# Kernel tuning notes

Hardware: AMD Instinct MI355X
Metric: run time of the kernel (lower is better)

## Reference

```python
import jax, jax.numpy as jnp
import numpy as np

N = 20000      # atoms
E = 320000     # edges
F = 128        # node_size (hard-pinned by split(128) / expand to 384)
RBF = 20
RC = 5.0
ITERS = 3
NM = 64        # molecules in batch


def setup_inputs() -> dict:
    key = jax.random.key(0)
    ks = iter(jax.random.split(key, 64))
    def nrm(shape, scale=0.05):
        return jax.random.normal(next(ks), shape, dtype=jnp.float32) * scale
    inp = {}
    inp["z"] = jax.random.randint(next(ks), (N,), 0, 119)
    inp["graph"] = jax.random.randint(next(ks), (E, 2), 0, N)
    inp["edges_dist"] = jax.random.uniform(next(ks), (E,), minval=0.5, maxval=RC, dtype=jnp.float32)
    sense = jax.random.normal(next(ks), (E, 3), dtype=jnp.float32)
    inp["edges_sense"] = sense / jnp.linalg.norm(sense, axis=1, keepdims=True)
    inp["graph_idx"] = jnp.sort(jax.random.randint(next(ks), (N,), 0, NM))
    # parameters (stacked over ITERS message/update blocks)
    inp["emb"] = nrm((119, F), 1.0)
    inp["mw1"] = nrm((ITERS, F, F)); inp["mb1"] = nrm((ITERS, F))
    inp["mw2"] = nrm((ITERS, 3 * F, F)); inp["mb2"] = nrm((ITERS, 3 * F))
    inp["ew"] = nrm((ITERS, 3 * F, RBF)); inp["eb"] = nrm((ITERS, 3 * F))
    inp["uw"] = nrm((ITERS, F, F)); inp["vw"] = nrm((ITERS, F, F))
    inp["aw1"] = nrm((ITERS, F, 2 * F)); inp["ab1"] = nrm((ITERS, F))
    inp["aw2"] = nrm((ITERS, 3 * F, F)); inp["ab2"] = nrm((ITERS, 3 * F))
    inp["ow1"] = nrm((F, F)); inp["ob1"] = nrm((F,))
    inp["ow2"] = nrm((1, F)); inp["ob2"] = nrm((1,))
    return inp


def reference(z, graph, edges_dist, edges_sense, graph_idx,
              emb, mw1, mb1, mw2, mb2, ew, eb,
              uw, vw, aw1, ab1, aw2, ab2, ow1, ob1, ow2, ob2):
    src = graph[:, 0]   # scatter target (index_add index)
    dst = graph[:, 1]   # gather source (neighbour)
    s = emb[z]                                  # [N, F]
    v = jnp.zeros((N, 3, F), dtype=s.dtype)     # [N, 3, F]
    # edge-level precompute (same every iteration)
    n = jnp.arange(1, RBF + 1, dtype=jnp.float32)
    d = edges_dist[:, None]
    rbf = jnp.sin(n * jnp.pi * d / RC) / d                              # [E, RBF]
    cut = 0.5 * (jnp.cos(jnp.pi * edges_dist / RC) + 1.0) * (edges_dist < RC)  # [E]
    for i in range(ITERS):
        # --- Message block ---
        a = jax.nn.silu(s @ mw1[i].T + mb1[i]) @ mw2[i].T + mb2[i]      # [N, 3F]
        dist_rep = (rbf @ ew[i].T + eb[i]) * cut[:, None]               # [E, 3F]
        res = a[dst] * dist_rep                                         # [E, 3F]
        rv, rs, rd = res[:, :F], res[:, F:2 * F], res[:, 2 * F:]
        resv = v[dst] * rv[:, None, :] + edges_sense[:, :, None] * rd[:, None, :]  # [E,3,F]
        s = s + 2.0 * jax.ops.segment_sum(rs, src, num_segments=N)
        v = v + 2.0 * jax.ops.segment_sum(resv, src, num_segments=N)
        # --- Update block ---
        Uv = v @ uw[i].T                                                # [N,3,F]
        Vv = v @ vw[i].T
        h = jnp.concatenate([s, jnp.linalg.norm(Vv, axis=1)], axis=-1)  # [N, 2F]
        a2 = jax.nn.silu(h @ aw1[i].T + ab1[i]) @ aw2[i].T + ab2[i]     # [N, 3F]
        avv, asv, ass = a2[:, :F], a2[:, F:2 * F], a2[:, 2 * F:]
        s = s + ass + asv * jnp.sum(Uv * Vv, axis=1)
        v = v + avv[:, None, :] * Uv
    out = jax.nn.silu(s @ ow1.T + ob1) @ ow2.T + ob2                    # [N, 1]
    return jax.ops.segment_sum(out, graph_idx, num_segments=NM)         # [NM, 1]
```

## Files before the change

kernel.cpp:

```cpp
#include <hip/hip_runtime.h>
#include <math.h>

#define NN 20000
#define NE 320000
#define FD 128
#define RBFN 20
#define RC_ 5.0f
#define NITER 3
#define NMOL 64
#define F3 384
#define F2 256
#define PI_ 3.14159265358979323846f
#define KB 128
#define LPAD 8
#define SDS 392
#define BM2 32

typedef __attribute__((ext_vector_type(8))) short  bf16x8;
typedef __attribute__((ext_vector_type(4))) float  floatx4;
typedef unsigned short u16;
typedef unsigned int   u32;

__device__ __forceinline__ u16 f2b(float x) {
    union { float f; unsigned int u; } v; v.f = x;
    unsigned int u = v.u;
    return (u16)((u + 0x7fffu + ((u >> 16) & 1u)) >> 16);
}
__device__ __forceinline__ float b2f(u16 x) {
    union { unsigned int u; float f; } v; v.u = ((unsigned int)x) << 16;
    return v.f;
}
__device__ __forceinline__ float blo(u32 w) {
    union { unsigned int u; float f; } v; v.u = w << 16; return v.f;
}
__device__ __forceinline__ float bhi(u32 w) {
    union { unsigned int u; float f; } v; v.u = w & 0xffff0000u; return v.f;
}
__device__ __forceinline__ u32 pack2(float a, float b) {
    return (u32)f2b(a) | ((u32)f2b(b) << 16);
}

__global__ __launch_bounds__(256) void init_all_kernel(
    const float* s0, int n0, const float* s1, int n1, const float* s2, int n2,
    const float* s3, int n3, const float* s4, int n4, const float* s5, int n5,
    const float* s6, int n6, u16* __restrict__ wdst,
    const float* __restrict__ ew, u16* __restrict__ ewb,
    const int* __restrict__ z, const float* __restrict__ emb,
    float* __restrict__ s, u16* __restrict__ sbf,
    float* __restrict__ v_a, int* __restrict__ v_pk_i, int* __restrict__ cnt)
{
    int idx = blockIdx.x * 256 + threadIdx.x;
    if (idx < NN * F3) v_a[idx] = 0.f;
    if (idx < NN * F3 / 2) v_pk_i[idx] = 0;
    if (idx < NN) cnt[idx] = 0;
    if (idx < NN * FD) {
        int n = idx >> 7, f = idx & 127;
        float v = emb[z[n] * FD + f];
        s[idx] = v; sbf[idx] = f2b(v);
    }
    if (idx < NITER * F3 * 32) {
        int k = idx & 31;
        int row = idx >> 5;
        ewb[idx] = (k < RBFN) ? f2b(ew[row * RBFN + k]) : (u16)0;
    }
    {
        int w = idx;
        u16* dst = wdst;
        if (w < n0) { dst[w] = f2b(s0[w]); return; } w -= n0; dst += n0;
        if (w < n1) { dst[w] = f2b(s1[w]); return; } w -= n1; dst += n1;
        if (w < n2) { dst[w] = f2b(s2[w]); return; } w -= n2; dst += n2;
        if (w < n3) { dst[w] = f2b(s3[w]); return; } w -= n3; dst += n3;
        if (w < n4) { dst[w] = f2b(s4[w]); return; } w -= n4; dst += n4;
        if (w < n5) { dst[w] = f2b(s5[w]); return; } w -= n5; dst += n5;
        if (w < n6) { dst[w] = f2b(s6[w]); }
    }
}

__global__ __launch_bounds__(256) void csr_count_kernel(const int* __restrict__ graph,
    int* __restrict__ cnt)
{
    int e = blockIdx.x * 256 + threadIdx.x;
    if (e >= NE) return;
    atomicAdd(&cnt[graph[2 * e]], 1);
}

__global__ __launch_bounds__(1024) void csr_scan_kernel(const int* __restrict__ cnt,
    int* __restrict__ row_ptr, int* __restrict__ cursor)
{
    __shared__ int sd[1024];
    int tid = threadIdx.x;
    const int chunk = (NN + 1023) / 1024;
    int start = tid * chunk;
    int end = start + chunk; if (end > NN) end = NN;
    int sum = 0;
    for (int j = start; j < end; j++) sum += cnt[j];
    sd[tid] = sum;
    __syncthreads();
    for (int off = 1; off < 1024; off <<= 1) {
        int v = 0;
        if (tid >= off) v = sd[tid - off];
        __syncthreads();
        if (tid >= off) sd[tid] += v;
        __syncthreads();
    }
    int run = (tid == 0) ? 0 : sd[tid - 1];
    for (int j = start; j < end; j++) {
        row_ptr[j] = run;
        cursor[j]  = run;
        run += cnt[j];
    }
    if (tid == 0) row_ptr[NN] = NE;
}

__global__ __launch_bounds__(256) void csr_scatter_kernel(const int* __restrict__ graph,
    int* __restrict__ cursor, int* __restrict__ edge_list)
{
    int e = blockIdx.x * 256 + threadIdx.x;
    if (e >= NE) return;
    int p = atomicAdd(&cursor[graph[2 * e]], 1);
    edge_list[p] = e;
}

__global__ __launch_bounds__(256) void edge_stream_kernel(
    const int* __restrict__ edge_list, const int* __restrict__ graph,
    const float* __restrict__ dist, const float* __restrict__ sense,
    u16* __restrict__ rbf_bf, float* __restrict__ cut_p,
    float* __restrict__ sense_p, int* __restrict__ dst_p)
{
    int j = blockIdx.x * 256 + threadIdx.x;
    if (j >= NE) return;
    int e = edge_list[j];
    float d = dist[e];
    float inv = 1.f / d;
    float base = PI_ * d / RC_;
    float s1, c1;
    __sincosf(base, &s1, &c1);
    float twoc = c1 + c1;
    u16 tmp[32];
    float sprev = 0.f, scur = s1;
    #pragma unroll
    for (int k = 0; k < RBFN; k++) {
        tmp[k] = f2b(scur * inv);
        float snext = twoc * scur - sprev;
        sprev = scur; scur = snext;
    }
    #pragma unroll
    for (int k = RBFN; k < 32; k++) tmp[k] = 0;
    u16* rb = rbf_bf + (size_t)j * 32;
    #pragma unroll
    for (int x = 0; x < 32; x += 8)
        *(bf16x8*)&rb[x] = *(const bf16x8*)&tmp[x];
    cut_p[j] = 0.5f * (c1 + 1.f) * (d < RC_ ? 1.f : 0.f);
    dst_p[j] = graph[2 * e + 1];
    sense_p[3 * j + 0] = sense[3 * e + 0];
    sense_p[3 * j + 1] = sense[3 * e + 1];
    sense_p[3 * j + 2] = sense[3 * e + 2];
}

template<int K1, bool PACK>
__global__ __launch_bounds__(256) void mlp_kernel(const u16* __restrict__ A,
    const u16* __restrict__ W1, const float* __restrict__ b1,
    const u16* __restrict__ W2, const float* __restrict__ b2,
    u16* __restrict__ Ob, int M)
{
    __shared__ u16 As[64][KB + LPAD];
    __shared__ u16 Ws[128][KB + LPAD];
    u16 (*T)[KB + LPAD] = &Ws[64];
    const int bm = blockIdx.x * 64;
    const int tid = threadIdx.x;
    const int wave = tid >> 6, lane = tid & 63;
    const int wm  = (wave >> 1) * 32;
    const int wn1 = (wave & 1) * 64;
    const int wn  = (wave & 1) * 32;
    const int quad = lane >> 4, lr = lane & 15;
    const int r = tid >> 2, q = tid & 3;

    floatx4 acc1[2][4];
    #pragma unroll
    for (int i = 0; i < 2; i++)
        #pragma unroll
        for (int j = 0; j < 4; j++) acc1[i][j] = (floatx4)0.f;

    for (int ko = 0; ko < K1; ko += KB) {
        {
            int gm = bm + r;
            u16* dA = &As[r][q * 32];
            if (gm < M) {
                const u16* ap = A + (size_t)gm * K1 + ko + q * 32;
                #pragma unroll
                for (int x = 0; x < 32; x += 8)
                    *(bf16x8*)&dA[x] = *(const bf16x8*)(ap + x);
            } else {
                #pragma unroll
                for (int x = 0; x < 32; x += 8)
                    *(bf16x8*)&dA[x] = (bf16x8)0;
            }
            #pragma unroll
            for (int h = 0; h < 2; h++) {
                int wr = r + h * 64;
                const u16* wp = W1 + (size_t)wr * K1 + ko + q * 32;
                u16* dW = &Ws[wr][q * 32];
                #pragma unroll
                for (int x = 0; x < 32; x += 8)
                    *(bf16x8*)&dW[x] = *(const bf16x8*)(wp + x);
            }
        }
        __syncthreads();
        #pragma unroll
        for (int kk = 0; kk < KB; kk += 32) {
            bf16x8 a0 = *(const bf16x8*)&As[wm + lr     ][kk + quad * 8];
            bf16x8 a1 = *(const bf16x8*)&As[wm + 16 + lr][kk + quad * 8];
            #pragma unroll
            for (int j = 0; j < 4; j++) {
                bf16x8 b = *(const bf16x8*)&Ws[wn1 + j * 16 + lr][kk + quad * 8];
                acc1[0][j] = __builtin_amdgcn_mfma_f32_16x16x32_bf16(a0, b, acc1[0][j], 0, 0, 0);
                acc1[1][j] = __builtin_amdgcn_mfma_f32_16x16x32_bf16(a1, b, acc1[1][j], 0, 0, 0);
            }
        }
        __syncthreads();
    }
    #pragma unroll
    for (int i = 0; i < 2; i++) {
        #pragma unroll
        for (int j = 0; j < 4; j++) {
            int col = wn1 + j * 16 + lr;
            float bb = b1[col];
            #pragma unroll
            for (int rr = 0; rr < 4; rr++) {
                int row = wm + i * 16 + quad * 4 + rr;
                float v = acc1[i][j][rr] + bb;
                v = v / (1.f + __expf(-v));
                T[row][col] = f2b(v);
            }
        }
    }

    for (int c0 = 0; c0 < F3; c0 += 64) {
        {
            const u16* wp = W2 + (size_t)(c0 + r) * KB + q * 32;
            u16* dW = &Ws[r][q * 32];
            #pragma unroll
            for (int x = 0; x < 32; x += 8)
                *(bf16x8*)&dW[x] = *(const bf16x8*)(wp + x);
        }
        __syncthreads();
        floatx4 acc2[2][2];
        #pragma unroll
        for (int i = 0; i < 2; i++)
            #pragma unroll
            for (int j = 0; j < 2; j++) acc2[i][j] = (floatx4)0.f;
        #pragma unroll
        for (int kk = 0; kk < KB; kk += 32) {
            bf16x8 a0 = *(const bf16x8*)&T[wm + lr     ][kk + quad * 8];
            bf16x8 a1 = *(const bf16x8*)&T[wm + 16 + lr][kk + quad * 8];
            bf16x8 b0 = *(const bf16x8*)&Ws[wn + lr     ][kk + quad * 8];
            bf16x8 b1 = *(const bf16x8*)&Ws[wn + 16 + lr][kk + quad * 8];
            acc2[0][0] = __builtin_amdgcn_mfma_f32_16x16x32_bf16(a0, b0, acc2[0][0], 0, 0, 0);
            acc2[0][1] = __builtin_amdgcn_mfma_f32_16x16x32_bf16(a0, b1, acc2[0][1], 0, 0, 0);
            acc2[1][0] = __builtin_amdgcn_mfma_f32_16x16x32_bf16(a1, b0, acc2[1][0], 0, 0, 0);
            acc2[1][1] = __builtin_amdgcn_mfma_f32_16x16x32_bf16(a1, b1, acc2[1][1], 0, 0, 0);
        }
        #pragma unroll
        for (int i = 0; i < 2; i++) {
            #pragma unroll
            for (int j = 0; j < 2; j++) {
                int gn = c0 + wn + j * 16 + lr;
                float bb = b2[gn];
                #pragma unroll
                for (int rr = 0; rr < 4; rr++) {
                    int gm = bm + wm + i * 16 + quad * 4 + rr;
                    if (gm < M) {
                        u16 val = f2b(acc2[i][j][rr] + bb);
                        if (PACK) {
                            int off = (gn < 256) ? ((gn & 127) * 2 + (gn >> 7))
                                                 : (256 + (gn & 127));
                            Ob[(size_t)gm * F3 + off] = val;
                        } else {
                            Ob[(size_t)gm * F3 + gn] = val;
                        }
                    }
                }
            }
        }
        __syncthreads();
    }
}

__global__ __launch_bounds__(256) void gemm_uv(const u16* __restrict__ A,
    const u16* __restrict__ Wu, const u16* __restrict__ Wv,
    u16* __restrict__ U, u16* __restrict__ V, int M)
{
    __shared__ u16 As[64][KB + LPAD];
    __shared__ u16 Bu[64][KB + LPAD];
    __shared__ u16 Bv[64][KB + LPAD];
    const int bm = blockIdx.x * 64;
    const int tid = threadIdx.x;
    const int r = tid >> 2;
    const int q = tid & 3;
    const int wave = tid >> 6;
    const int lane = tid & 63;
    const int wm = (wave >> 1) * 32;
    const int wn = (wave & 1) * 32;
    const int quad = lane >> 4;
    const int lr = lane & 15;

    {
        int gm = bm + r;
        u16* dA = &As[r][q * 32];
        if (gm < M) {
            const u16* ap = A + (size_t)gm * KB + q * 32;
            #pragma unroll
            for (int x = 0; x < 32; x += 8)
                *(bf16x8*)&dA[x] = *(const bf16x8*)(ap + x);
        } else {
            #pragma unroll
            for (int x = 0; x < 32; x += 8)
                *(bf16x8*)&dA[x] = (bf16x8)0;
        }
    }

    #pragma unroll
    for (int bn = 0; bn < FD; bn += 64) {
        {
            int gn = bn + r;
            const u16* up = Wu + (size_t)gn * KB + q * 32;
            const u16* vp = Wv + (size_t)gn * KB + q * 32;
            u16* dU = &Bu[r][q * 32];
            u16* dV = &Bv[r][q * 32];
            #pragma unroll
            for (int x = 0; x < 32; x += 8) {
                *(bf16x8*)&dU[x] = *(const bf16x8*)(up + x);
                *(bf16x8*)&dV[x] = *(const bf16x8*)(vp + x);
            }
        }
        __syncthreads();
        floatx4 au[2][2], av[2][2];
        #pragma unroll
        for (int i = 0; i < 2; i++)
            #pragma unroll
            for (int j = 0; j < 2; j++) { au[i][j] = (floatx4)0.f; av[i][j] = (floatx4)0.f; }
        #pragma unroll
        for (int kk = 0; kk < KB; kk += 32) {
            bf16x8 a0 = *(const bf16x8*)&As[wm + lr     ][kk + quad * 8];
            bf16x8 a1 = *(const bf16x8*)&As[wm + 16 + lr][kk + quad * 8];
            bf16x8 u0 = *(const bf16x8*)&Bu[wn + lr     ][kk + quad * 8];
            bf16x8 u1 = *(const bf16x8*)&Bu[wn + 16 + lr][kk + quad * 8];
            bf16x8 v0 = *(const bf16x8*)&Bv[wn + lr     ][kk + quad * 8];
            bf16x8 v1 = *(const bf16x8*)&Bv[wn + 16 + lr][kk + quad * 8];
            au[0][0] = __builtin_amdgcn_mfma_f32_16x16x32_bf16(a0, u0, au[0][0], 0, 0, 0);
            au[0][1] = __builtin_amdgcn_mfma_f32_16x16x32_bf16(a0, u1, au[0][1], 0, 0, 0);
            au[1][0] = __builtin_amdgcn_mfma_f32_16x16x32_bf16(a1, u0, au[1][0], 0, 0, 0);
            au[1][1] = __builtin_amdgcn_mfma_f32_16x16x32_bf16(a1, u1, au[1][1], 0, 0, 0);
            av[0][0] = __builtin_amdgcn_mfma_f32_16x16x32_bf16(a0, v0, av[0][0], 0, 0, 0);
            av[0][1] = __builtin_amdgcn_mfma_f32_16x16x32_bf16(a0, v1, av[0][1], 0, 0, 0);
            av[1][0] = __builtin_amdgcn_mfma_f32_16x16x32_bf16(a1, v0, av[1][0], 0, 0, 0);
            av[1][1] = __builtin_amdgcn_mfma_f32_16x16x32_bf16(a1, v1, av[1][1], 0, 0, 0);
        }
        #pragma unroll
        for (int i = 0; i < 2; i++) {
            #pragma unroll
            for (int j = 0; j < 2; j++) {
                int gn = bn + wn + j * 16 + lr;
                #pragma unroll
                for (int rr = 0; rr < 4; rr++) {
                    int gm = bm + wm + i * 16 + quad * 4 + rr;
                    if (gm < M) {
                        U[(size_t)gm * FD + gn] = f2b(au[i][j][rr]);
                        V[(size_t)gm * FD + gn] = f2b(av[i][j][rr]);
                    }
                }
            }
        }
        __syncthreads();
    }
}

__global__ __launch_bounds__(256) void edge_mfma_kernel(
    const u16* __restrict__ rbf_bf, const float* __restrict__ cut_p,
    const float* __restrict__ sense_p, const int* __restrict__ dst_p,
    const u16* __restrict__ ewb, const float* __restrict__ eb,
    const u16* __restrict__ a_pk, const float* __restrict__ s_in,
    const float* __restrict__ v_in, const u16* __restrict__ v_pk,
    const int* __restrict__ row_ptr,
    float* __restrict__ s_out, u16* __restrict__ s_obf,
    float* __restrict__ v_out, u16* __restrict__ v_obf)
{
    __shared__ u16   sdrep[16 * SDS];
    __shared__ float scut[16];
    __shared__ float ssen[16][4];
    __shared__ int   sdst[16];
    __shared__ float red[4 * 128];

    const int n = blockIdx.x;
    const int tid = threadIdx.x;
    const int wave = tid >> 6;
    const int lane = tid & 63;
    const int quad = lane >> 4;
    const int lr = lane & 15;
    const int f = tid & 127;
    const int half = tid >> 7;

    int beg = row_ptr[n], end = row_ptr[n + 1];
    float accs = 0.f, accv0 = 0.f, accv1 = 0.f, accv2 = 0.f;

    for (int t0 = beg; t0 < end; t0 += 16) {
        int cnt = end - t0; if (cnt > 16) cnt = 16;
        __syncthreads();
        if (tid < 16) {
            scut[tid] = (tid < cnt) ? cut_p[t0 + tid] : 0.f;
            sdst[tid] = (tid < cnt) ? dst_p[t0 + tid] : 0;
        }
        if (tid >= 64 && tid < 64 + 3 * cnt) {
            int x = tid - 64;
            ssen[x / 3][x % 3] = sense_p[3 * t0 + x];
        }
        bf16x8 afrag;
        int ge = t0 + lr;
        if (ge < end) afrag = *(const bf16x8*)&rbf_bf[(size_t)ge * 32 + quad * 8];
        else          afrag = (bf16x8)0;
        floatx4 dacc[6];
        #pragma unroll
        for (int nt = 0; nt < 6; nt++) {
            int nrow = (wave * 6 + nt) * 16 + lr;
            bf16x8 bfrag = *(const bf16x8*)&ewb[(size_t)nrow * 32 + quad * 8];
            dacc[nt] = __builtin_amdgcn_mfma_f32_16x16x32_bf16(afrag, bfrag, (floatx4)0.f, 0, 0, 0);
        }
        __syncthreads();
        #pragma unroll
        for (int nt = 0; nt < 6; nt++) {
            int ncol = (wave * 6 + nt) * 16 + lr;
            float ebn = eb[ncol];
            #pragma unroll
            for (int rr = 0; rr < 4; rr++) {
                int e = quad * 4 + rr;
                sdrep[e * SDS + ncol] = f2b((dacc[nt][rr] + ebn) * scut[e]);
            }
        }
        __syncthreads();
        int nh = cnt - half * 8; if (nh > 8) nh = 8;
        for (int k = 0; k < nh; k++) {
            int e = half * 8 + k;
            int dst = sdst[e];
            const u16* sr = &sdrep[e * SDS];
            float drv = b2f(sr[f]);
            float drs = b2f(sr[FD + f]);
            float drd = b2f(sr[2 * FD + f]);
            const u16* ar = a_pk + (size_t)dst * F3;
            u32 ap = *(const u32*)(ar + f * 2);
            float rv = b2f((u16)(ap & 0xffff)) * drv;
            float rs = b2f((u16)(ap >> 16))    * drs;
            float rd = b2f(ar[256 + f])        * drd;
            accs += rs;
            const u16* vr = v_pk + (size_t)dst * F3;
            u32 vp = *(const u32*)(vr + f * 2);
            accv0 += b2f((u16)(vp & 0xffff)) * rv + ssen[e][0] * rd;
            accv1 += b2f((u16)(vp >> 16))    * rv + ssen[e][1] * rd;
            accv2 += b2f(vr[256 + f])        * rv + ssen[e][2] * rd;
        }
    }
    __syncthreads();
    if (half == 1) {
        red[f] = accs; red[128 + f] = accv0; red[256 + f] = accv1; red[384 + f] = accv2;
    }
    __syncthreads();
    if (half == 0) {
        accs  += red[f];       accv0 += red[128 + f];
        accv1 += red[256 + f]; accv2 += red[384 + f];
        int nb = n * FD + f;
        float so = s_in[nb] + 2.f * accs;
        s_out[nb] = so; s_obf[nb] = f2b(so);
        int vb = n * F3 + f;
        float w0 = v_in[vb]           + 2.f * accv0;
        float w1 = v_in[vb + FD]      + 2.f * accv1;
        float w2 = v_in[vb + 2 * FD]  + 2.f * accv2;
        v_out[vb]          = w0; v_obf[vb]          = f2b(w0);
        v_out[vb + FD]     = w1; v_obf[vb + FD]     = f2b(w1);
        v_out[vb + 2 * FD] = w2; v_obf[vb + 2 * FD] = f2b(w2);
    }
}

template<bool LAST>
__global__ __launch_bounds__(256) void mlp2_update_next_kernel(
    const u16* __restrict__ sbf_mid, const float* __restrict__ s_mid,
    const float* __restrict__ v_mid,
    const u16* __restrict__ Uv, const u16* __restrict__ Vv,
    const u16* __restrict__ W1, const float* __restrict__ b1,
    const u16* __restrict__ W2, const float* __restrict__ b2,
    float* __restrict__ s_out,
    float* __restrict__ v_out, u16* __restrict__ v_pk,
    const u16* __restrict__ N_W1, const float* __restrict__ N_b1,
    const u16* __restrict__ N_W2, const float* __restrict__ N_b2,
    u16* __restrict__ a_pk,
    const u16* __restrict__ H_W1, const float* __restrict__ H_b1,
    const float* __restrict__ ow2, const float* __restrict__ ob2,
    float* __restrict__ nodeval, int M)
{
    __shared__ u16 As[BM2][KB + LPAD];
    __shared__ u16 Ws[128][KB + LPAD];
    u16 (*T)[KB + LPAD] = &Ws[64];
    const int bm = blockIdx.x * BM2;
    const int tid = threadIdx.x;
    const int wave = tid >> 6, lane = tid & 63;
    const int wrow = (wave >> 1) * 16;
    const int wn1  = (wave & 1) * 64;
    const int wn   = (wave & 1) * 32;
    const int quad = lane >> 4, lr = lane & 15;
    const int r = tid >> 2, q = tid & 3;
    const int r3 = tid >> 3, c16 = (tid & 7) * 16;

    floatx4 acc1[4];
    #pragma unroll
    for (int j = 0; j < 4; j++) acc1[j] = (floatx4)0.f;

    {
        int gm = bm + r3;
        u16* dA = &As[r3][c16];
        if (gm < M) {
            const u16* ap = sbf_mid + (size_t)gm * FD + c16;
            *(bf16x8*)&dA[0] = *(const bf16x8*)(ap);
            *(bf16x8*)&dA[8] = *(const bf16x8*)(ap + 8);
        } else {
            *(bf16x8*)&dA[0] = (bf16x8)0;
            *(bf16x8*)&dA[8] = (bf16x8)0;
        }
        #pragma unroll
        for (int h = 0; h < 2; h++) {
            int wr = r + h * 64;
            const u16* wp = W1 + (size_t)wr * F2 + q * 32;
            u16* dW = &Ws[wr][q * 32];
            #pragma unroll
            for (int x = 0; x < 32; x += 8)
                *(bf16x8*)&dW[x] = *(const bf16x8*)(wp + x);
        }
    }
    __syncthreads();
    #pragma unroll
    for (int kk = 0; kk < KB; kk += 32) {
        bf16x8 a0 = *(const bf16x8*)&As[wrow + lr][kk + quad * 8];
        #pragma unroll
        for (int j = 0; j < 4; j++) {
            bf16x8 b = *(const bf16x8*)&Ws[wn1 + j * 16 + lr][kk + quad * 8];
            acc1[j] = __builtin_amdgcn_mfma_f32_16x16x32_bf16(a0, b, acc1[j], 0, 0, 0);
        }
    }
    __syncthreads();
    {
        int gm = bm + r3;
        u16* dA = &As[r3][c16];
        if (gm < M) {
            const u16* vvp = Vv + (size_t)gm * F3 + c16;
            #pragma unroll
            for (int t = 0; t < 2; t++) {
                bf16x8 c0 = *(const bf16x8*)(vvp + t * 8);
                bf16x8 c1 = *(const bf16x8*)(vvp + FD + t * 8);
                bf16x8 c2 = *(const bf16x8*)(vvp + 2 * FD + t * 8);
                #pragma unroll
                for (int x = 0; x < 8; x++) {
                    float a = b2f((u16)c0[x]);
                    float b = b2f((u16)c1[x]);
                    float c = b2f((u16)c2[x]);
                    dA[t * 8 + x] = f2b(sqrtf(a * a + b * b + c * c));
                }
            }
        } else {
            *(bf16x8*)&dA[0] = (bf16x8)0;
            *(bf16x8*)&dA[8] = (bf16x8)0;
        }
        #pragma unroll
        for (int h = 0; h < 2; h++) {
            int wr = r + h * 64;
            const u16* wp = W1 + (size_t)wr * F2 + KB + q * 32;
            u16* dW = &Ws[wr][q * 32];
            #pragma unroll
            for (int x = 0; x < 32; x += 8)
                *(bf16x8*)&dW[x] = *(const bf16x8*)(wp + x);
        }
    }
    __syncthreads();
    #pragma unroll
    for (int kk = 0; kk < KB; kk += 32) {
        bf16x8 a0 = *(const bf16x8*)&As[wrow + lr][kk + quad * 8];
        #pragma unroll
        for (int j = 0; j < 4; j++) {
            bf16x8 b = *(const bf16x8*)&Ws[wn1 + j * 16 + lr][kk + quad * 8];
            acc1[j] = __builtin_amdgcn_mfma_f32_16x16x32_bf16(a0, b, acc1[j], 0, 0, 0);
        }
    }
    __syncthreads();
    #pragma unroll
    for (int j = 0; j < 4; j++) {
        int col = wn1 + j * 16 + lr;
        float bb = b1[col];
        #pragma unroll
        for (int rr = 0; rr < 4; rr++) {
            int row = wrow + quad * 4 + rr;
            float v = acc1[j][rr] + bb;
            v = v / (1.f + __expf(-v));
            T[row][col] = f2b(v);
        }
    }

    float avvr[2][4], asvr[2][4];
    #pragma unroll
    for (int pp = 0; pp < 6; pp++) {
        const int part  = pp / 3;
        const int piece = pp % 3;
        const int c0 = piece * 128 + part * 64;
        {
            const u16* wp = W2 + (size_t)(c0 + r) * KB + q * 32;
            u16* dW = &Ws[r][q * 32];
            #pragma unroll
            for (int x = 0; x < 32; x += 8)
                *(bf16x8*)&dW[x] = *(const bf16x8*)(wp + x);
        }
        __syncthreads();
        floatx4 acc2[2];
        #pragma unroll
        for (int j = 0; j < 2; j++) acc2[j] = (floatx4)0.f;
        #pragma unroll
        for (int kk = 0; kk < KB; kk += 32) {
            bf16x8 a0 = *(const bf16x8*)&T[wrow + lr][kk + quad * 8];
            bf16x8 b0 = *(const bf16x8*)&Ws[wn + lr     ][kk + quad * 8];
            bf16x8 b1 = *(const bf16x8*)&Ws[wn + 16 + lr][kk + quad * 8];
            acc2[0] = __builtin_amdgcn_mfma_f32_16x16x32_bf16(a0, b0, acc2[0], 0, 0, 0);
            acc2[1] = __builtin_amdgcn_mfma_f32_16x16x32_bf16(a0, b1, acc2[1], 0, 0, 0);
        }
        if (piece == 0) {
            #pragma unroll
            for (int j = 0; j < 2; j++) {
                int gn = c0 + wn + j * 16 + lr;
                float bb = b2[gn];
                #pragma unroll
                for (int rr = 0; rr < 4; rr++)
                    avvr[j][rr] = acc2[j][rr] + bb;
            }
        } else if (piece == 1) {
            #pragma unroll
            for (int j = 0; j < 2; j++) {
                int gn = c0 + wn + j * 16 + lr;
                float bb = b2[gn];
                #pragma unroll
                for (int rr = 0; rr < 4; rr++)
                    asvr[j][rr] = acc2[j][rr] + bb;
            }
        } else {
            #pragma unroll
            for (int j = 0; j < 2; j++) {
                int gn = c0 + wn + j * 16 + lr;
                int f  = gn - 256;
                float bb = b2[gn];
                #pragma unroll
                for (int rr = 0; rr < 4; rr++) {
                    int row = wrow + quad * 4 + rr;
                    int gm = bm + row;
                    if (gm < M) {
                        float ass = acc2[j][rr] + bb;
                        float asv = asvr[j][rr];
                        float avv = avvr[j][rr];
                        int vb = gm * F3 + f;
                        float u0 = b2f(Uv[vb]);
                        float u1 = b2f(Uv[vb + FD]);
                        float u2 = b2f(Uv[vb + 2 * FD]);
                        float w0 = b2f(Vv[vb]);
                        float w1 = b2f(Vv[vb + FD]);
                        float w2 = b2f(Vv[vb + 2 * FD]);
                        float dot = u0 * w0 + u1 * w1 + u2 * w2;
                        int nb = gm * FD + f;
                        float so = s_mid[nb] + ass + asv * dot;
                        s_out[nb] = so;
                        As[row][f] = f2b(so);
                        float y0 = v_mid[vb]          + avv * u0;
                        float y1 = v_mid[vb + FD]     + avv * u1;
                        float y2 = v_mid[vb + 2 * FD] + avv * u2;
                        v_out[vb]          = y0;
                        v_out[vb + FD]     = y1;
                        v_out[vb + 2 * FD] = y2;
                        char* vpb = (char*)v_pk + (size_t)gm * (2 * F3);
                        *(u32*)(vpb + 4 * f) = pack2(y0, y1);
                        *(u16*)(vpb + 512 + 2 * f) = f2b(y2);
                    } else {
                        As[row][f] = 0;
                    }
                }
            }
        }
        __syncthreads();
    }

    if constexpr (!LAST) {
        {
            #pragma unroll
            for (int h = 0; h < 2; h++) {
                int wr = r + h * 64;
                const u16* wp = N_W1 + (size_t)wr * KB + q * 32;
                u16* dW = &Ws[wr][q * 32];
                #pragma unroll
                for (int x = 0; x < 32; x += 8)
                    *(bf16x8*)&dW[x] = *(const bf16x8*)(wp + x);
            }
        }
        __syncthreads();
        #pragma unroll
        for (int j = 0; j < 4; j++) acc1[j] = (floatx4)0.f;
        #pragma unroll
        for (int kk = 0; kk < KB; kk += 32) {
            bf16x8 a0 = *(const bf16x8*)&As[wrow + lr][kk + quad * 8];
            #pragma unroll
            for (int j = 0; j < 4; j++) {
                bf16x8 b = *(const bf16x8*)&Ws[wn1 + j * 16 + lr][kk + quad * 8];
                acc1[j] = __builtin_amdgcn_mfma_f32_16x16x32_bf16(a0, b, acc1[j], 0, 0, 0);
            }
        }
        __syncthreads();
        #pragma unroll
        for (int j = 0; j < 4; j++) {
            int col = wn1 + j * 16 + lr;
            float bb = N_b1[col];
            #pragma unroll
            for (int rr = 0; rr < 4; rr++) {
                int row = wrow + quad * 4 + rr;
                float v = acc1[j][rr] + bb;
                v = v / (1.f + __expf(-v));
                T[row][col] = f2b(v);
            }
        }
        for (int pp = 0; pp < 6; pp++) {
            const int c0 = pp * 64;
            {
                const u16* wp = N_W2 + (size_t)(c0 + r) * KB + q * 32;
                u16* dW = &Ws[r][q * 32];
                #pragma unroll
                for (int x = 0; x < 32; x += 8)
                    *(bf16x8*)&dW[x] = *(const bf16x8*)(wp + x);
            }
            __syncthreads();
            floatx4 acc2[2];
            #pragma unroll
            for (int j = 0; j < 2; j++) acc2[j] = (floatx4)0.f;
            #pragma unroll
            for (int kk = 0; kk < KB; kk += 32) {
                bf16x8 a0 = *(const bf16x8*)&T[wrow + lr][kk + quad * 8];
                bf16x8 b0 = *(const bf16x8*)&Ws[wn + lr     ][kk + quad * 8];
                bf16x8 b1 = *(const bf16x8*)&Ws[wn + 16 + lr][kk + quad * 8];
                acc2[0] = __builtin_amdgcn_mfma_f32_16x16x32_bf16(a0, b0, acc2[0], 0, 0, 0);
                acc2[1] = __builtin_amdgcn_mfma_f32_16x16x32_bf16(a0, b1, acc2[1], 0, 0, 0);
            }
            #pragma unroll
            for (int j = 0; j < 2; j++) {
                int gn = c0 + wn + j * 16 + lr;
                float bb = N_b2[gn];
                #pragma unroll
                for (int rr = 0; rr < 4; rr++) {
                    int gm = bm + wrow + quad * 4 + rr;
                    if (gm < M) {
                        u16 val = f2b(acc2[j][rr] + bb);
                        int off = (gn < 256) ? ((gn & 127) * 2 + (gn >> 7))
                                             : (256 + (gn & 127));
                        a_pk[(size_t)gm * F3 + off] = val;
                    }
                }
            }
            __syncthreads();
        }
    } else {
        {
            #pragma unroll
            for (int h = 0; h < 2; h++) {
                int wr = r + h * 64;
                const u16* wp = H_W1 + (size_t)wr * KB + q * 32;
                u16* dW = &Ws[wr][q * 32];
                #pragma unroll
                for (int x = 0; x < 32; x += 8)
                    *(bf16x8*)&dW[x] = *(const bf16x8*)(wp + x);
            }
        }
        __syncthreads();
        #pragma unroll
        for (int j = 0; j < 4; j++) acc1[j] = (floatx4)0.f;
        #pragma unroll
        for (int kk = 0; kk < KB; kk += 32) {
            bf16x8 a0 = *(const bf16x8*)&As[wrow + lr][kk + quad * 8];
            #pragma unroll
            for (int j = 0; j < 4; j++) {
                bf16x8 b = *(const bf16x8*)&Ws[wn1 + j * 16 + lr][kk + quad * 8];
                acc1[j] = __builtin_amdgcn_mfma_f32_16x16x32_bf16(a0, b, acc1[j], 0, 0, 0);
            }
        }
        __syncthreads();
        float* ow2s = (float*)&As[0][0];
        if (tid < KB) ow2s[tid] = ow2[tid];
        #pragma unroll
        for (int j = 0; j < 4; j++) {
            int col = wn1 + j * 16 + lr;
            float bb = H_b1[col];
            #pragma unroll
            for (int rr = 0; rr < 4; rr++) {
                int row = wrow + quad * 4 + rr;
                float v = acc1[j][rr] + bb;
                v = v / (1.f + __expf(-v));
                T[row][col] = f2b(v);
            }
        }
        __syncthreads();
        int nl = tid >> 3, seg = tid & 7;
        float v = 0.f;
        #pragma unroll
        for (int x = 0; x < 16; x++) {
            int col = seg * 16 + x;
            v += b2f(T[nl][col]) * ow2s[col];
        }
        v += __shfl_down(v, 4);
        v += __shfl_down(v, 2);
        v += __shfl_down(v, 1);
        if (seg == 0) {
            int gm = bm + nl;
            if (gm < M) nodeval[gm] = v + ob2[0];
        }
    }
}

__global__ __launch_bounds__(1024) void mol_reduce_kernel(const float* __restrict__ nodeval,
    const int* __restrict__ gidx, float* __restrict__ out)
{
    __shared__ float mol[NMOL];
    int tid = threadIdx.x;
    if (tid < NMOL) mol[tid] = 0.f;
    __syncthreads();
    int cur = -1; float acc = 0.f;
    for (int x = tid; x < NN; x += 1024) {
        int g = gidx[x];
        float v = nodeval[x];
        if (g != cur) {
            if (cur >= 0) atomicAdd(&mol[cur], acc);
            cur = g; acc = v;
        } else acc += v;
    }
    if (cur >= 0) atomicAdd(&mol[cur], acc);
    __syncthreads();
    if (tid < NMOL) out[tid] = mol[tid];
}

extern "C" void kernel_launch(void* const* d_in, const int* in_sizes, int n_in,
                              void* d_out, int out_size, void* d_ws, size_t ws_size,
                              hipStream_t stream)
{
    const int*   z     = (const int*)d_in[0];
    const int*   graph = (const int*)d_in[1];
    const float* dist  = (const float*)d_in[2];
    const float* sense = (const float*)d_in[3];
    const int*   gidx  = (const int*)d_in[4];
    const float* emb   = (const float*)d_in[5];
    const float* mw1   = (const float*)d_in[6];
    const float* mb1   = (const float*)d_in[7];
    const float* mw2   = (const float*)d_in[8];
    const float* mb2   = (const float*)d_in[9];
    const float* ew    = (const float*)d_in[10];
    const float* eb    = (const float*)d_in[11];
    const float* uw    = (const float*)d_in[12];
    const float* vw    = (const float*)d_in[13];
    const float* aw1   = (const float*)d_in[14];
    const float* ab1   = (const float*)d_in[15];
    const float* aw2   = (const float*)d_in[16];
    const float* ab2   = (const float*)d_in[17];
    const float* ow1   = (const float*)d_in[18];
    const float* ob1   = (const float*)d_in[19];
    const float* ow2   = (const float*)d_in[20];
    const float* ob2   = (const float*)d_in[21];
    float* out = (float*)d_out;

    float* W = (float*)d_ws;
    float* s_a    = W; W += (size_t)NN * FD;
    float* s_b    = W; W += (size_t)NN * FD;
    float* v_a    = W; W += (size_t)NN * F3;
    float* v_b    = W; W += (size_t)NN * F3;
    float* cut_p  = W; W += (size_t)NE;
    float* sns_p  = W; W += (size_t)NE * 3;
    float* nodeval= W; W += (size_t)NN;
    u16* U = (u16*)W;
    u16* sbf_a = U; U += (size_t)NN * FD;
    u16* sbf_b = U; U += (size_t)NN * FD;
    u16* vbf_b = U; U += (size_t)NN * F3;
    u16* a_pk  = U; U += (size_t)NN * F3;
    u16* v_pk  = U; U += (size_t)NN * F3;
    u16* h_bf  = U; U += (size_t)NN * F2;
    u16* a2_bf = U; U += (size_t)NN * F3;
    u16* Uv_bf = U; U += (size_t)NN * F3;
    u16* Vv_bf = U; U += (size_t)NN * F3;
    u16* rbf_bf= U; U += (size_t)NE * 32;
    u16* ewb   = U; U += (size_t)NITER * F3 * 32;
    u16* wb    = U; U += 557056;
    int* ip = (int*)U;
    int* row_ptr   = ip; ip += NN + 1;
    int* cnt       = ip; ip += NN;
    int* cursor    = ip; ip += NN;
    int* edge_list = ip; ip += NE;
    int* dst_p     = ip; ip += NE;

    u16* wb_mw1 = wb;
    u16* wb_mw2 = wb + 49152;
    u16* wb_uw  = wb + 196608;
    u16* wb_vw  = wb + 245760;
    u16* wb_aw1 = wb + 294912;
    u16* wb_aw2 = wb + 393216;
    u16* wb_ow1 = wb + 540672;

    const int TB = 256;
    dim3 b256(TB);

    init_all_kernel<<<dim3((NN * F3 + TB - 1) / TB), b256, 0, stream>>>(
        mw1, 49152, mw2, 147456, uw, 49152, vw, 49152, aw1, 98304, aw2, 147456,
        ow1, 16384, wb, ew, ewb, z, emb, s_a, sbf_a, v_a, (int*)v_pk, cnt);
    csr_count_kernel<<<dim3((NE + TB - 1) / TB), b256, 0, stream>>>(graph, cnt);
    csr_scan_kernel<<<dim3(1), dim3(1024), 0, stream>>>(cnt, row_ptr, cursor);
    csr_scatter_kernel<<<dim3((NE + TB - 1) / TB), b256, 0, stream>>>(graph, cursor, edge_list);
    edge_stream_kernel<<<dim3((NE + TB - 1) / TB), b256, 0, stream>>>(
        edge_list, graph, dist, sense, rbf_bf, cut_p, sns_p, dst_p);

    dim3 gM((NN + 63) / 64);
    dim3 gM2((NN + BM2 - 1) / BM2);
    dim3 gUV((3 * NN + 63) / 64);

    mlp_kernel<128, true><<<gM, b256, 0, stream>>>(sbf_a,
        wb_mw1, mb1, wb_mw2, mb2, a_pk, NN);

    for (int i = 0; i < NITER; i++) {
        edge_mfma_kernel<<<dim3(NN), b256, 0, stream>>>(
            rbf_bf, cut_p, sns_p, dst_p,
            ewb + (size_t)i * F3 * 32, eb + (size_t)i * F3,
            a_pk, s_a, v_a, v_pk, row_ptr, s_b, sbf_b, v_b, vbf_b);
        gemm_uv<<<gUV, b256, 0, stream>>>(vbf_b, wb_uw + (size_t)i * FD * FD,
            wb_vw + (size_t)i * FD * FD, Uv_bf, Vv_bf, 3 * NN);
        if (i < NITER - 1) {
            mlp2_update_next_kernel<false><<<gM2, b256, 0, stream>>>(
                sbf_b, s_b, v_b, Uv_bf, Vv_bf,
                wb_aw1 + (size_t)i * FD * F2, ab1 + (size_t)i * FD,
                wb_aw2 + (size_t)i * F3 * FD, ab2 + (size_t)i * F3,
                s_a, v_a, v_pk,
                wb_mw1 + (size_t)(i + 1) * FD * FD, mb1 + (size_t)(i + 1) * FD,
                wb_mw2 + (size_t)(i + 1) * F3 * FD, mb2 + (size_t)(i + 1) * F3, a_pk,
                nullptr, nullptr, nullptr, nullptr, nullptr, NN);
        } else {
            mlp2_update_next_kernel<true><<<gM2, b256, 0, stream>>>(
                sbf_b, s_b, v_b, Uv_bf, Vv_bf,
                wb_aw1 + (size_t)i * FD * F2, ab1 + (size_t)i * FD,
                wb_aw2 + (size_t)i * F3 * FD, ab2 + (size_t)i * F3,
                s_a, v_a, v_pk,
                nullptr, nullptr, nullptr, nullptr, nullptr,
                wb_ow1, ob1, ow2, ob2, nodeval, NN);
        }
    }

    mol_reduce_kernel<<<dim3(1), dim3(1024), 0, stream>>>(nodeval, gidx, out);
}
```

Baseline: 855.1 us.

## Halve row tile in mlp1 and gemm_uv; fuse molecule reduction via atomics

The first MLP kernel and the U/V GEMM now use 32-row tiles instead of 64, so each wave covers 16 rows. That doubles the number of blocks and lowers per-block register and LDS use, at the cost of reloading weight tiles more often. The separate single-block molecule-reduction kernel is removed. The final update kernel now atomically adds each node's value into the output per molecule, with the output zeroed in the init kernel. This saves a launch and a serial reduction but adds per-node global atomics and makes the float summation order nondeterministic.

Measured after the change: 934.5 us. 9.3% more time.

```diff
diff --git a/kernel.cpp b/kernel.cpp
--- a/kernel.cpp
+++ b/kernel.cpp
@@ -47,12 +47,14 @@
     const float* __restrict__ ew, u16* __restrict__ ewb,
     const int* __restrict__ z, const float* __restrict__ emb,
     float* __restrict__ s, u16* __restrict__ sbf,
-    float* __restrict__ v_a, int* __restrict__ v_pk_i, int* __restrict__ cnt)
+    float* __restrict__ v_a, int* __restrict__ v_pk_i, int* __restrict__ cnt,
+    float* __restrict__ out)
 {
     int idx = blockIdx.x * 256 + threadIdx.x;
     if (idx < NN * F3) v_a[idx] = 0.f;
     if (idx < NN * F3 / 2) v_pk_i[idx] = 0;
     if (idx < NN) cnt[idx] = 0;
+    if (idx < NMOL) out[idx] = 0.f;
     if (idx < NN * FD) {
         int n = idx >> 7, f = idx & 127;
         float v = emb[z[n] * FD + f];
@@ -157,85 +159,74 @@
     sense_p[3 * j + 2] = sense[3 * e + 2];
 }
 
-template<int K1, bool PACK>
-__global__ __launch_bounds__(256) void mlp_kernel(const u16* __restrict__ A,
+__global__ __launch_bounds__(256) void mlp1_kernel(const u16* __restrict__ A,
     const u16* __restrict__ W1, const float* __restrict__ b1,
     const u16* __restrict__ W2, const float* __restrict__ b2,
     u16* __restrict__ Ob, int M)
 {
-    __shared__ u16 As[64][KB + LPAD];
+    __shared__ u16 As[BM2][KB + LPAD];
     __shared__ u16 Ws[128][KB + LPAD];
     u16 (*T)[KB + LPAD] = &Ws[64];
-    const int bm = blockIdx.x * 64;
+    const int bm = blockIdx.x * BM2;
     const int tid = threadIdx.x;
     const int wave = tid >> 6, lane = tid & 63;
-    const int wm  = (wave >> 1) * 32;
-    const int wn1 = (wave & 1) * 64;
-    const int wn  = (wave & 1) * 32;
+    const int wrow = (wave >> 1) * 16;
+    const int wn1  = (wave & 1) * 64;
+    const int wn   = (wave & 1) * 32;
     const int quad = lane >> 4, lr = lane & 15;
     const int r = tid >> 2, q = tid & 3;
-
-    floatx4 acc1[2][4];
-    #pragma unroll
-    for (int i = 0; i < 2; i++)
-        #pragma unroll
-        for (int j = 0; j < 4; j++) acc1[i][j] = (floatx4)0.f;
-
-    for (int ko = 0; ko < K1; ko += KB) {
-        {
-            int gm = bm + r;
-            u16* dA = &As[r][q * 32];
-            if (gm < M) {
-                const u16* ap = A + (size_t)gm * K1 + ko + q * 32;
-                #pragma unroll
-                for (int x = 0; x < 32; x += 8)
-                    *(bf16x8*)&dA[x] = *(const bf16x8*)(ap + x);
-            } else {
-                #pragma unroll
-                for (int x = 0; x < 32; x += 8)
-                    *(bf16x8*)&dA[x] = (bf16x8)0;
-            }
-            #pragma unroll
-            for (int h = 0; h < 2; h++) {
-                int wr = r + h * 64;
-                const u16* wp = W1 + (size_t)wr * K1 + ko + q * 32;
-                u16* dW = &Ws[wr][q * 32];
-                #pragma unroll
-                for (int x = 0; x < 32; x += 8)
-                    *(bf16x8*)&dW[x] = *(const bf16x8*)(wp + x);
-            }
-        }
-        __syncthreads();
-        #pragma unroll
-        for (int kk = 0; kk < KB; kk += 32) {
-            bf16x8 a0 = *(const bf16x8*)&As[wm + lr     ][kk + quad * 8];
-            bf16x8 a1 = *(const bf16x8*)&As[wm + 16 + lr][kk + quad * 8];
-            #pragma unroll
-            for (int j = 0; j < 4; j++) {
-                bf16x8 b = *(const bf16x8*)&Ws[wn1 + j * 16 + lr][kk + quad * 8];
-                acc1[0][j] = __builtin_amdgcn_mfma_f32_16x16x32_bf16(a0, b, acc1[0][j], 0, 0, 0);
-                acc1[1][j] = __builtin_amdgcn_mfma_f32_16x16x32_bf16(a1, b, acc1[1][j], 0, 0, 0);
-            }
-        }
-        __syncthreads();
-    }
-    #pragma unroll
-    for (int i = 0; i < 2; i++) {
+    const int r3 = tid >> 3, c16 = (tid & 7) * 16;
+
+    floatx4 acc1[4];
+    #pragma unroll
+    for (int j = 0; j < 4; j++) acc1[j] = (floatx4)0.f;
+
+    {
+        int gm = bm + r3;
+        u16* dA = &As[r3][c16];
+        if (gm < M) {
+            const u16* ap = A + (size_t)gm * KB + c16;
+            *(bf16x8*)&dA[0] = *(const bf16x8*)(ap);
+            *(bf16x8*)&dA[8] = *(const bf16x8*)(ap + 8);
+        } else {
+            *(bf16x8*)&dA[0] = (bf16x8)0;
+            *(bf16x8*)&dA[8] = (bf16x8)0;
+        }
+        #pragma unroll
+        for (int h = 0; h < 2; h++) {
+            int wr = r + h * 64;
+            const u16* wp = W1 + (size_t)wr * KB + q * 32;
+            u16* dW = &Ws[wr][q * 32];
+            #pragma unroll
+            for (int x = 0; x < 32; x += 8)
+                *(bf16x8*)&dW[x] = *(const bf16x8*)(wp + x);
+        }
+    }
+    __syncthreads();
+    #pragma unroll
+    for (int kk = 0; kk < KB; kk += 32) {
+        bf16x8 a0 = *(const bf16x8*)&As[wrow + lr][kk + quad * 8];
         #pragma unroll
         for (int j = 0; j < 4; j++) {
-            int col = wn1 + j * 16 + lr;
-            float bb = b1[col];
-            #pragma unroll
-            for (int rr = 0; rr < 4; rr++) {
-                int row = wm + i * 16 + quad * 4 + rr;
-                float v = acc1[i][j][rr] + bb;
-                v = v / (1.f + __expf(-v));
-                T[row][col] = f2b(v);
-            }
-        }
-    }
-
-    for (int c0 = 0; c0 < F3; c0 += 64) {
+            bf16x8 b = *(const bf16x8*)&Ws[wn1 + j * 16 + lr][kk + quad * 8];
+            acc1[j] = __builtin_amdgcn_mfma_f32_16x16x32_bf16(a0, b, acc1[j], 0, 0, 0);
+        }
+    }
+    __syncthreads();
+    #pragma unroll
+    for (int j = 0; j < 4; j++) {
+        int col = wn1 + j * 16 + lr;
+        float bb = b1[col];
+        #pragma unroll
+        for (int rr = 0; rr < 4; rr++) {
+            int row = wrow + quad * 4 + rr;
+            float v = acc1[j][rr] + bb;
+            v = v / (1.f + __expf(-v));
+            T[row][col] = f2b(v);
+        }
+    }
+    for (int pp = 0; pp < 6; pp++) {
+        const int c0 = pp * 64;
         {
             const u16* wp = W2 + (size_t)(c0 + r) * KB + q * 32;
             u16* dW = &Ws[r][q * 32];
@@ -244,41 +235,29 @@
                 *(bf16x8*)&dW[x] = *(const bf16x8*)(wp + x);
         }
         __syncthreads();
-        floatx4 acc2[2][2];
-        #pragma unroll
-        for (int i = 0; i < 2; i++)
-            #pragma unroll
-            for (int j = 0; j < 2; j++) acc2[i][j] = (floatx4)0.f;
+        floatx4 acc2[2];
+        #pragma unroll
+        for (int j = 0; j < 2; j++) acc2[j] = (floatx4)0.f;
         #pragma unroll
         for (int kk = 0; kk < KB; kk += 32) {
-            bf16x8 a0 = *(const bf16x8*)&T[wm + lr     ][kk + quad * 8];
-            bf16x8 a1 = *(const bf16x8*)&T[wm + 16 + lr][kk + quad * 8];
+            bf16x8 a0 = *(const bf16x8*)&T[wrow + lr][kk + quad * 8];
             bf16x8 b0 = *(const bf16x8*)&Ws[wn + lr     ][kk + quad * 8];
             bf16x8 b1 = *(const bf16x8*)&Ws[wn + 16 + lr][kk + quad * 8];
-            acc2[0][0] = __builtin_amdgcn_mfma_f32_16x16x32_bf16(a0, b0, acc2[0][0], 0, 0, 0);
-            acc2[0][1] = __builtin_amdgcn_mfma_f32_16x16x32_bf16(a0, b1, acc2[0][1], 0, 0, 0);
-            acc2[1][0] = __builtin_amdgcn_mfma_f32_16x16x32_bf16(a1, b0, acc2[1][0], 0, 0, 0);
-            acc2[1][1] = __builtin_amdgcn_mfma_f32_16x16x32_bf16(a1, b1, acc2[1][1], 0, 0, 0);
-        }
-        #pragma unroll
-        for (int i = 0; i < 2; i++) {
-            #pragma unroll
-            for (int j = 0; j < 2; j++) {
-                int gn = c0 + wn + j * 16 + lr;
-                float bb = b2[gn];
-                #pragma unroll
-                for (int rr = 0; rr < 4; rr++) {
-                    int gm = bm + wm + i * 16 + quad * 4 + rr;
-                    if (gm < M) {
-                        u16 val = f2b(acc2[i][j][rr] + bb);
-                        if (PACK) {
-                            int off = (gn < 256) ? ((gn & 127) * 2 + (gn >> 7))
-                                                 : (256 + (gn & 127));
-                            Ob[(size_t)gm * F3 + off] = val;
-                        } else {
-                            Ob[(size_t)gm * F3 + gn] = val;
-                        }
-                    }
+            acc2[0] = __builtin_amdgcn_mfma_f32_16x16x32_bf16(a0, b0, acc2[0], 0, 0, 0);
+            acc2[1] = __builtin_amdgcn_mfma_f32_16x16x32_bf16(a0, b1, acc2[1], 0, 0, 0);
+        }
+        #pragma unroll
+        for (int j = 0; j < 2; j++) {
+            int gn = c0 + wn + j * 16 + lr;
+            float bb = b2[gn];
+            #pragma unroll
+            for (int rr = 0; rr < 4; rr++) {
+                int gm = bm + wrow + quad * 4 + rr;
+                if (gm < M) {
+                    u16 val = f2b(acc2[j][rr] + bb);
+                    int off = (gn < 256) ? ((gn & 127) * 2 + (gn >> 7))
+                                         : (256 + (gn & 127));
+                    Ob[(size_t)gm * F3 + off] = val;
                 }
             }
         }
@@ -290,32 +269,31 @@
     const u16* __restrict__ Wu, const u16* __restrict__ Wv,
     u16* __restrict__ U, u16* __restrict__ V, int M)
 {
-    __shared__ u16 As[64][KB + LPAD];
+    __shared__ u16 As[BM2][KB + LPAD];
     __shared__ u16 Bu[64][KB + LPAD];
     __shared__ u16 Bv[64][KB + LPAD];
-    const int bm = blockIdx.x * 64;
+    const int bm = blockIdx.x * BM2;
     const int tid = threadIdx.x;
     const int r = tid >> 2;
     const int q = tid & 3;
+    const int r3 = tid >> 3, c16 = (tid & 7) * 16;
     const int wave = tid >> 6;
     const int lane = tid & 63;
-    const int wm = (wave >> 1) * 32;
+    const int wrow = (wave >> 1) * 16;
     const int wn = (wave & 1) * 32;
     const int quad = lane >> 4;
     const int lr = lane & 15;
 
     {
-        int gm = bm + r;
-        u16* dA = &As[r][q * 32];
+        int gm = bm + r3;
+        u16* dA = &As[r3][c16];
         if (gm < M) {
-            const u16* ap = A + (size_t)gm * KB + q * 32;
-            #pragma unroll
-            for (int x = 0; x < 32; x += 8)
-                *(bf16x8*)&dA[x] = *(const bf16x8*)(ap + x);
+            const u16* ap = A + (size_t)gm * KB + c16;
+            *(bf16x8*)&dA[0] = *(const bf16x8*)(ap);
+            *(bf16x8*)&dA[8] = *(const bf16x8*)(ap + 8);
         } else {
-            #pragma unroll
-            for (int x = 0; x < 32; x += 8)
-                *(bf16x8*)&dA[x] = (bf16x8)0;
+            *(bf16x8*)&dA[0] = (bf16x8)0;
+            *(bf16x8*)&dA[8] = (bf16x8)0;
         }
     }
 
@@ -334,40 +312,30 @@
             }
         }
         __syncthreads();
-        floatx4 au[2][2], av[2][2];
-        #pragma unroll
-        for (int i = 0; i < 2; i++)
-            #pragma unroll
-            for (int j = 0; j < 2; j++) { au[i][j] = (floatx4)0.f; av[i][j] = (floatx4)0.f; }
+        floatx4 au[2], av[2];
+        #pragma unroll
+        for (int j = 0; j < 2; j++) { au[j] = (floatx4)0.f; av[j] = (floatx4)0.f; }
         #pragma unroll
         for (int kk = 0; kk < KB; kk += 32) {
-            bf16x8 a0 = *(const bf16x8*)&As[wm + lr     ][kk + quad * 8];
-            bf16x8 a1 = *(const bf16x8*)&As[wm + 16 + lr][kk + quad * 8];
+            bf16x8 a0 = *(const bf16x8*)&As[wrow + lr][kk + quad * 8];
             bf16x8 u0 = *(const bf16x8*)&Bu[wn + lr     ][kk + quad * 8];
             bf16x8 u1 = *(const bf16x8*)&Bu[wn + 16 + lr][kk + quad * 8];
             bf16x8 v0 = *(const bf16x8*)&Bv[wn + lr     ][kk + quad * 8];
             bf16x8 v1 = *(const bf16x8*)&Bv[wn + 16 + lr][kk + quad * 8];
-            au[0][0] = __builtin_amdgcn_mfma_f32_16x16x32_bf16(a0, u0, au[0][0], 0, 0, 0);
-            au[0][1] = __builtin_amdgcn_mfma_f32_16x16x32_bf16(a0, u1, au[0][1], 0, 0, 0);
-            au[1][0] = __builtin_amdgcn_mfma_f32_16x16x32_bf16(a1, u0, au[1][0], 0, 0, 0);
-            au[1][1] = __builtin_amdgcn_mfma_f32_16x16x32_bf16(a1, u1, au[1][1], 0, 0, 0);
-            av[0][0] = __builtin_amdgcn_mfma_f32_16x16x32_bf16(a0, v0, av[0][0], 0, 0, 0);
-            av[0][1] = __builtin_amdgcn_mfma_f32_16x16x32_bf16(a0, v1, av[0][1], 0, 0, 0);
-            av[1][0] = __builtin_amdgcn_mfma_f32_16x16x32_bf16(a1, v0, av[1][0], 0, 0, 0);
-            av[1][1] = __builtin_amdgcn_mfma_f32_16x16x32_bf16(a1, v1, av[1][1], 0, 0, 0);
-        }
-        #pragma unroll
-        for (int i = 0; i < 2; i++) {
-            #pragma unroll
-            for (int j = 0; j < 2; j++) {
-                int gn = bn + wn + j * 16 + lr;
-                #pragma unroll
-                for (int rr = 0; rr < 4; rr++) {
-                    int gm = bm + wm + i * 16 + quad * 4 + rr;
-                    if (gm < M) {
-                        U[(size_t)gm * FD + gn] = f2b(au[i][j][rr]);
-                        V[(size_t)gm * FD + gn] = f2b(av[i][j][rr]);
-                    }
+            au[0] = __builtin_amdgcn_mfma_f32_16x16x32_bf16(a0, u0, au[0], 0, 0, 0);
+            au[1] = __builtin_amdgcn_mfma_f32_16x16x32_bf16(a0, u1, au[1], 0, 0, 0);
+            av[0] = __builtin_amdgcn_mfma_f32_16x16x32_bf16(a0, v0, av[0], 0, 0, 0);
+            av[1] = __builtin_amdgcn_mfma_f32_16x16x32_bf16(a0, v1, av[1], 0, 0, 0);
+        }
+        #pragma unroll
+        for (int j = 0; j < 2; j++) {
+            int gn = bn + wn + j * 16 + lr;
+            #pragma unroll
+            for (int rr = 0; rr < 4; rr++) {
+                int gm = bm + wrow + quad * 4 + rr;
+                if (gm < M) {
+                    U[(size_t)gm * FD + gn] = f2b(au[j][rr]);
+                    V[(size_t)gm * FD + gn] = f2b(av[j][rr]);
                 }
             }
         }
@@ -493,7 +461,7 @@
     u16* __restrict__ a_pk,
     const u16* __restrict__ H_W1, const float* __restrict__ H_b1,
     const float* __restrict__ ow2, const float* __restrict__ ob2,
-    float* __restrict__ nodeval, int M)
+    const int* __restrict__ gidx, float* __restrict__ outp, int M)
 {
     __shared__ u16 As[BM2][KB + LPAD];
     __shared__ u16 Ws[128][KB + LPAD];
@@ -814,30 +782,9 @@
         v += __shfl_down(v, 1);
         if (seg == 0) {
             int gm = bm + nl;
-            if (gm < M) nodeval[gm] = v + ob2[0];
-        }
-    }
-}
-
-__global__ __launch_bounds__(1024) void mol_reduce_kernel(const float* __restrict__ nodeval,
-    const int* __restrict__ gidx, float* __restrict__ out)
-{
-    __shared__ float mol[NMOL];
-    int tid = threadIdx.x;
-    if (tid < NMOL) mol[tid] = 0.f;
-    __syncthreads();
-    int cur = -1; float acc = 0.f;
-    for (int x = tid; x < NN; x += 1024) {
-        int g = gidx[x];
-        float v = nodeval[x];
-        if (g != cur) {
-            if (cur >= 0) atomicAdd(&mol[cur], acc);
-            cur = g; acc = v;
-        } else acc += v;
-    }
-    if (cur >= 0) atomicAdd(&mol[cur], acc);
-    __syncthreads();
-    if (tid < NMOL) out[tid] = mol[tid];
+            if (gm < M) atomicAdd(&outp[gidx[gm]], v + ob2[0]);
+        }
+    }
 }
 
 extern "C" void kernel_launch(void* const* d_in, const int* in_sizes, int n_in,
@@ -909,18 +856,17 @@
 
     init_all_kernel<<<dim3((NN * F3 + TB - 1) / TB), b256, 0, stream>>>(
         mw1, 49152, mw2, 147456, uw, 49152, vw, 49152, aw1, 98304, aw2, 147456,
-        ow1, 16384, wb, ew, ewb, z, emb, s_a, sbf_a, v_a, (int*)v_pk, cnt);
+        ow1, 16384, wb, ew, ewb, z, emb, s_a, sbf_a, v_a, (int*)v_pk, cnt, out);
     csr_count_kernel<<<dim3((NE + TB - 1) / TB), b256, 0, stream>>>(graph, cnt);
     csr_scan_kernel<<<dim3(1), dim3(1024), 0, stream>>>(cnt, row_ptr, cursor);
     csr_scatter_kernel<<<dim3((NE + TB - 1) / TB), b256, 0, stream>>>(graph, cursor, edge_list);
     edge_stream_kernel<<<dim3((NE + TB - 1) / TB), b256, 0, stream>>>(
         edge_list, graph, dist, sense, rbf_bf, cut_p, sns_p, dst_p);
 
-    dim3 gM((NN + 63) / 64);
     dim3 gM2((NN + BM2 - 1) / BM2);
-    dim3 gUV((3 * NN + 63) / 64);
-
-    mlp_kernel<128, true><<<gM, b256, 0, stream>>>(sbf_a,
+    dim3 gUV((3 * NN + BM2 - 1) / BM2);
+
+    mlp1_kernel<<<gM2, b256, 0, stream>>>(sbf_a,
         wb_mw1, mb1, wb_mw2, mb2, a_pk, NN);
 
     for (int i = 0; i < NITER; i++) {
@@ -938,7 +884,7 @@
                 s_a, v_a, v_pk,
                 wb_mw1 + (size_t)(i + 1) * FD * FD, mb1 + (size_t)(i + 1) * FD,
                 wb_mw2 + (size_t)(i + 1) * F3 * FD, mb2 + (size_t)(i + 1) * F3, a_pk,
-                nullptr, nullptr, nullptr, nullptr, nullptr, NN);
+                nullptr, nullptr, nullptr, nullptr, nullptr, nullptr, NN);
         } else {
             mlp2_update_next_kernel<true><<<gM2, b256, 0, stream>>>(
                 sbf_b, s_b, v_b, Uv_bf, Vv_bf,
@@ -946,9 +892,7 @@
                 wb_aw2 + (size_t)i * F3 * FD, ab2 + (size_t)i * F3,
                 s_a, v_a, v_pk,
                 nullptr, nullptr, nullptr, nullptr, nullptr,
-                wb_ow1, ob1, ow2, ob2, nodeval, NN);
-        }
-    }
-
-    mol_reduce_kernel<<<dim3(1), dim3(1024), 0, stream>>>(nodeval, gidx, out);
-}
+                wb_ow1, ob1, ow2, ob2, gidx, out, NN);
+        }
+    }
+}
```
